# Kernel tuning notes

Hardware: AMD Instinct MI355X
Metric: run time of the kernel (lower is better)

The kernel has to match this reference:

```python
import jax, jax.numpy as jnp
import numpy as np

EPS = 0.05
N = 33554432  # 2**25 annotation steps


def setup_inputs() -> dict:
    key = jax.random.key(0)
    # categories in 1..5 (cat==0 is a no-op skip in the original loop; excluding it
    # keeps the output length static at N+1)
    annotation_series = jax.random.randint(key, (N,), 1, 6, dtype=jnp.int64 if jax.config.jax_enable_x64 else jnp.int32)
    # learned scalar weights of the six Linear(1,1,bias=False) layers, at their init constants
    return {
        "annotation_series": annotation_series,
        "origin_w": jnp.asarray(0.0, jnp.float32),
        "big_decrease_w": jnp.asarray(-0.3, jnp.float32),
        "decrease_w": jnp.asarray(-0.1, jnp.float32),
        "same_w": jnp.asarray(0.0, jnp.float32),
        "increase_w": jnp.asarray(0.1, jnp.float32),
        "big_increase_w": jnp.asarray(0.3, jnp.float32),
    }


def _change_table(origin_w, bd, d, s, inc, bi):
    sg = jax.lax.stop_gradient  # clamp bounds came from .item() in torch -> detached
    c1 = jnp.minimum(bd, sg(jnp.minimum(0.0, d))) - EPS                 # big decrease
    c2 = jnp.clip(d, sg(bd) + EPS, 0.0 - EPS)                           # decrease
    c3 = s                                                              # same
    c4 = jnp.clip(inc, 0.0 + EPS, sg(bi) - EPS)                         # increase
    c5 = jnp.maximum(bi, sg(jnp.maximum(0.0, inc)) + EPS)               # big increase
    zero = jnp.zeros_like(c1)  # cat 0 unused (inputs restricted to 1..5)
    return jnp.stack([zero, c1, c2, c3, c4, c5])  # [6]


def reference(annotation_series, origin_w, big_decrease_w, decrease_w, same_w, increase_w, big_increase_w):
    table = _change_table(origin_w, big_decrease_w, decrease_w, same_w, increase_w, big_increase_w)
    changes = table[annotation_series]                    # [N] gather from 6-entry LUT
    series = origin_w + jnp.cumsum(changes)               # [N] inclusive prefix sum
    return jnp.concatenate([origin_w[None], series])      # [N+1]
```

## Files before the change

kernel.cpp:

```cpp
#include <hip/hip_runtime.h>

#define EPS_C 0.05f
#define BLOCK 256
#define SUBT 2
#define CHUNK (SUBT * 4096)
#define CHUNK2 2048

typedef int i4 __attribute__((ext_vector_type(4)));

__device__ __forceinline__ void build_table(const float* bd_p, const float* d_p,
                                            const float* s_p, const float* inc_p,
                                            const float* bi_p, float* cs) {
  if (threadIdx.x == 0) {
    float bd = *bd_p, d = *d_p, s = *s_p, inc = *inc_p, bi = *bi_p;
    cs[0] = 0.0f;
    cs[1] = fminf(bd, fminf(0.0f, d)) - EPS_C;
    cs[2] = fminf(fmaxf(d, bd + EPS_C), -EPS_C);
    cs[3] = s;
    cs[4] = fminf(fmaxf(inc, EPS_C), bi - EPS_C);
    cs[5] = fmaxf(bi, fmaxf(0.0f, inc) + EPS_C);
    cs[6] = 0.0f; cs[7] = 0.0f;
  }
}

__global__ __launch_bounds__(BLOCK) void k_reduce_pack(
    const int* __restrict__ ann, const float* bd, const float* d,
    const float* s, const float* inc, const float* bi,
    uint2* __restrict__ packed, float* __restrict__ coarse,
    float* __restrict__ fine) {
  __shared__ float cs[8];
  __shared__ float wsum[SUBT * 4];
  build_table(bd, d, s, inc, bi, cs);
  __syncthreads();

  const int b = blockIdx.x, t = threadIdx.x;
  const int lane = t & 63, wid = t >> 6;
  const i4* in4 = (const i4*)(ann + (size_t)b * CHUNK);

#pragma unroll
  for (int j = 0; j < SUBT; ++j) {
    unsigned int w0 = 0u, w1 = 0u;
    float sum = 0.0f;
#pragma unroll
    for (int i = 0; i < 4; ++i) {
      i4 v = __builtin_nontemporal_load(&in4[j * 1024 + t * 4 + i]);
      sum += cs[v.x] + cs[v.y] + cs[v.z] + cs[v.w];
      unsigned int nib = (unsigned)v.x | ((unsigned)v.y << 4) |
                         ((unsigned)v.z << 8) | ((unsigned)v.w << 12);
      if (i < 2) w0 |= nib << ((i & 1) * 16);
      else       w1 |= nib << ((i & 1) * 16);
    }
    packed[(size_t)b * (SUBT * BLOCK) + j * BLOCK + t] = make_uint2(w0, w1);
#pragma unroll
    for (int off = 32; off >= 1; off >>= 1) sum += __shfl_down(sum, off, 64);
    if (lane == 0) {
      fine[b * (SUBT * 4) + j * 4 + wid] = sum;
      wsum[j * 4 + wid] = sum;
    }
  }
  __syncthreads();
  if (t == 0) {
    float tot = 0.0f;
#pragma unroll
    for (int i = 0; i < SUBT * 4; ++i) tot += wsum[i];
    coarse[b] = tot;
  }
}

__global__ __launch_bounds__(BLOCK) void k_scan_out(
    const unsigned short* __restrict__ uspack, const float* __restrict__ coarse,
    const float* __restrict__ fine, const float* __restrict__ origin,
    const float* bd, const float* d, const float* s, const float* inc,
    const float* bi, float* __restrict__ out, int nb2, int nbc) {
  __shared__ float cs[8];
  __shared__ float wsum[BLOCK / 64];
  __shared__ float s_base;
  build_table(bd, d, s, inc, bi, cs);
  __syncthreads();

  const int b2 = blockIdx.x, t = threadIdx.x;
  const int lane = t & 63, wid = t >> 6;
  const int cb = b2 >> 2;
  const int fcnt = 2 * (b2 & 3);

  unsigned short us0 = uspack[(size_t)b2 * 512 + t];
  unsigned short us1 = uspack[(size_t)b2 * 512 + 256 + t];

  float p = 0.0f;
  for (int i = t; i < cb; i += BLOCK) p += coarse[i];
  if (t < fcnt) p += fine[cb * 8 + t];
#pragma unroll
  for (int off = 32; off >= 1; off >>= 1) p += __shfl_down(p, off, 64);
  if (lane == 0) wsum[wid] = p;
  __syncthreads();
  if (t == 0) s_base = *origin + wsum[0] + wsum[1] + wsum[2] + wsum[3];
  __syncthreads();

  float carry = s_base;
  unsigned short usv[2] = {us0, us1};
#pragma unroll
  for (int r = 0; r < 2; ++r) {
    const unsigned short us = usv[r];
    float v0 = cs[us & 0xF], v1 = cs[(us >> 4) & 0xF];
    float v2 = cs[(us >> 8) & 0xF], v3 = cs[(us >> 12) & 0xF];
    float run = v0 + v1 + v2 + v3;

    float x = run;
#pragma unroll
    for (int off = 1; off < 64; off <<= 1) {
      float y = __shfl_up(x, off, 64);
      if (lane >= off) x += y;
    }
    __syncthreads();
    if (lane == 63) wsum[wid] = x;
    __syncthreads();
    float wexcl = 0.0f, tot = 0.0f;
#pragma unroll
    for (int i = 0; i < BLOCK / 64; ++i) {
      float wv = wsum[i];
      if (i < wid) wexcl += wv;
      tot += wv;
    }
    const float off0 = carry + wexcl + (x - run);

    float4 o;
    o.x = off0;
    o.y = off0 + v0;
    o.z = off0 + v0 + v1;
    o.w = off0 + v0 + v1 + v2;
    ((float4*)(out + (size_t)b2 * CHUNK2 + r * 1024))[t] = o;
    carry += tot;

    if (b2 == nb2 - 1 && t == BLOCK - 1 && r == 1)
      out[(size_t)nb2 * CHUNK2] = off0 + run;
  }
}

extern "C" void kernel_launch(void* const* d_in, const int* in_sizes, int n_in,
                              void* d_out, int out_size, void* d_ws, size_t ws_size,
                              hipStream_t stream) {
  const int*   ann    = (const int*)d_in[0];
  const float* origin = (const float*)d_in[1];
  const float* bd     = (const float*)d_in[2];
  const float* dw     = (const float*)d_in[3];
  const float* sw     = (const float*)d_in[4];
  const float* inc    = (const float*)d_in[5];
  const float* bi     = (const float*)d_in[6];
  float* out = (float*)d_out;

  const int N   = in_sizes[0];
  const int nbc = N / CHUNK;
  const int nb2 = N / CHUNK2;

  float* coarse = (float*)d_ws;
  float* fine   = (float*)((char*)d_ws + 65536);
  uint2* packed = (uint2*)((char*)d_ws + 262144);

  k_reduce_pack<<<nbc, BLOCK, 0, stream>>>(ann, bd, dw, sw, inc, bi,
                                           packed, coarse, fine);
  k_scan_out<<<nb2, BLOCK, 0, stream>>>((const unsigned short*)packed, coarse,
                                        fine, origin, bd, dw, sw, inc, bi,
                                        out, nb2, nbc);
}
```

Before: 264.3 us.

## Replace two-pass reduce/scan with single-pass decoupled look-back scan

Replaces the reduce-then-scan pair of kernels with one kernel that takes a dynamic block ticket, computes each 8192-element tile's sum, and publishes aggregate/inclusive descriptors for a wavefront-parallel decoupled look-back. Values stay in registers as packed nibbles, so the workspace round trip and the second pass over coarse/fine partial sums are gone. A small zeroing kernel clears descriptors and the ticket first. The cost is serial dependence through the look-back chain and spinning with s_sleep, plus reliance on agent-scope atomics for ordering.

```diff
diff --git a/kernel.cpp b/kernel.cpp
--- a/kernel.cpp
+++ b/kernel.cpp
@@ -2,137 +2,151 @@
 
 #define EPS_C 0.05f
 #define BLOCK 256
-#define SUBT 2
-#define CHUNK (SUBT * 4096)
-#define CHUNK2 2048
+#define CHUNK 8192
+#define FLAG_AGG 1ull
+#define FLAG_INC 2ull
 
 typedef int i4 __attribute__((ext_vector_type(4)));
+typedef float f4 __attribute__((ext_vector_type(4)));
 
-__device__ __forceinline__ void build_table(const float* bd_p, const float* d_p,
-                                            const float* s_p, const float* inc_p,
-                                            const float* bi_p, float* cs) {
-  if (threadIdx.x == 0) {
-    float bd = *bd_p, d = *d_p, s = *s_p, inc = *inc_p, bi = *bi_p;
-    cs[0] = 0.0f;
-    cs[1] = fminf(bd, fminf(0.0f, d)) - EPS_C;
-    cs[2] = fminf(fmaxf(d, bd + EPS_C), -EPS_C);
-    cs[3] = s;
-    cs[4] = fminf(fmaxf(inc, EPS_C), bi - EPS_C);
-    cs[5] = fmaxf(bi, fmaxf(0.0f, inc) + EPS_C);
-    cs[6] = 0.0f; cs[7] = 0.0f;
-  }
+__global__ void k_zero(unsigned long long* __restrict__ p, int n) {
+  int i = blockIdx.x * blockDim.x + threadIdx.x;
+  if (i < n) p[i] = 0ull;
 }
 
-__global__ __launch_bounds__(BLOCK) void k_reduce_pack(
-    const int* __restrict__ ann, const float* bd, const float* d,
-    const float* s, const float* inc, const float* bi,
-    uint2* __restrict__ packed, float* __restrict__ coarse,
-    float* __restrict__ fine) {
+__global__ __launch_bounds__(BLOCK) void k_scan_lookback(
+    const int* __restrict__ ann, const float* __restrict__ origin,
+    const float* __restrict__ bd, const float* __restrict__ d,
+    const float* __restrict__ s, const float* __restrict__ inc,
+    const float* __restrict__ bi, float* __restrict__ out,
+    unsigned long long* __restrict__ desc, unsigned int* __restrict__ ticket,
+    int nb) {
   __shared__ float cs[8];
-  __shared__ float wsum[SUBT * 4];
-  build_table(bd, d, s, inc, bi, cs);
+  __shared__ float wsum[4];
+  __shared__ float s_carry;
+  __shared__ int s_bid;
+
+  const int t = threadIdx.x;
+  const int lane = t & 63;
+  const int wid = t >> 6;
+
+  if (t == 0) {
+    float vbd = *bd, vd = *d, vs = *s, vi = *inc, vbi = *bi;
+    cs[0] = 0.0f;
+    cs[1] = fminf(vbd, fminf(0.0f, vd)) - EPS_C;
+    cs[2] = fminf(fmaxf(vd, vbd + EPS_C), -EPS_C);
+    cs[3] = vs;
+    cs[4] = fminf(fmaxf(vi, EPS_C), vbi - EPS_C);
+    cs[5] = fmaxf(vbi, fmaxf(0.0f, vi) + EPS_C);
+    cs[6] = 0.0f; cs[7] = 0.0f;
+    s_bid = (int)atomicAdd(ticket, 1u);
+  }
+  __syncthreads();
+  const int bid = s_bid;
+
+  unsigned pk0 = 0, pk1 = 0, pk2 = 0, pk3 = 0;
+  float tsum = 0.0f;
+  const i4* in4 = (const i4*)ann + ((size_t)bid * (CHUNK / 4) + wid * 512 + lane);
+#pragma unroll
+  for (int r = 0; r < 8; ++r) {
+    i4 v = __builtin_nontemporal_load(&in4[r * 64]);
+    tsum += cs[v.x] + cs[v.y] + cs[v.z] + cs[v.w];
+    unsigned nib = (unsigned)v.x | ((unsigned)v.y << 4) |
+                   ((unsigned)v.z << 8) | ((unsigned)v.w << 12);
+    unsigned sh = (unsigned)(r & 1) * 16u;
+    if (r < 2)      pk0 |= nib << sh;
+    else if (r < 4) pk1 |= nib << sh;
+    else if (r < 6) pk2 |= nib << sh;
+    else            pk3 |= nib << sh;
+  }
+#pragma unroll
+  for (int off = 32; off >= 1; off >>= 1) tsum += __shfl_xor(tsum, off, 64);
+  if (lane == 0) wsum[wid] = tsum;
   __syncthreads();
 
-  const int b = blockIdx.x, t = threadIdx.x;
-  const int lane = t & 63, wid = t >> 6;
-  const i4* in4 = (const i4*)(ann + (size_t)b * CHUNK);
-
+  if (wid == 0) {
+    const float total = wsum[0] + wsum[1] + wsum[2] + wsum[3];
+    float excl = 0.0f;
+    if (bid == 0) {
+      if (lane == 0) {
+        __hip_atomic_store(&desc[0],
+            (FLAG_INC << 32) | (unsigned long long)__float_as_uint(total),
+            __ATOMIC_RELEASE, __HIP_MEMORY_SCOPE_AGENT);
+        s_carry = 0.0f;
+      }
+    } else {
+      if (lane == 0)
+        __hip_atomic_store(&desc[bid],
+            (FLAG_AGG << 32) | (unsigned long long)__float_as_uint(total),
+            __ATOMIC_RELEASE, __HIP_MEMORY_SCOPE_AGENT);
+      int look = bid;
+      for (;;) {
+        const int idx = look - 1 - lane;
+        unsigned long long d0 = (idx >= 0)
+            ? __hip_atomic_load(&desc[idx], __ATOMIC_ACQUIRE, __HIP_MEMORY_SCOPE_AGENT)
+            : (FLAG_INC << 32);
+        const unsigned flag = (unsigned)(d0 >> 32);
+        const unsigned long long binc = __ballot(flag == 2u);
+        const unsigned long long bnone = __ballot(flag == 0u);
+        const int fi = binc ? (__ffsll((long long)binc) - 1) : 64;
+        const int fn = bnone ? (__ffsll((long long)bnone) - 1) : 64;
+        if (fi < fn) {
+          float v = (lane <= fi) ? __uint_as_float((unsigned)d0) : 0.0f;
 #pragma unroll
-  for (int j = 0; j < SUBT; ++j) {
-    unsigned int w0 = 0u, w1 = 0u;
-    float sum = 0.0f;
+          for (int off = 32; off >= 1; off >>= 1) v += __shfl_xor(v, off, 64);
+          excl += v;
+          break;
+        }
+        if (fn > 0) {
+          float v = (lane < fn) ? __uint_as_float((unsigned)d0) : 0.0f;
 #pragma unroll
-    for (int i = 0; i < 4; ++i) {
-      i4 v = __builtin_nontemporal_load(&in4[j * 1024 + t * 4 + i]);
-      sum += cs[v.x] + cs[v.y] + cs[v.z] + cs[v.w];
-      unsigned int nib = (unsigned)v.x | ((unsigned)v.y << 4) |
-                         ((unsigned)v.z << 8) | ((unsigned)v.w << 12);
-      if (i < 2) w0 |= nib << ((i & 1) * 16);
-      else       w1 |= nib << ((i & 1) * 16);
+          for (int off = 32; off >= 1; off >>= 1) v += __shfl_xor(v, off, 64);
+          excl += v;
+          look -= fn;
+        } else {
+          __builtin_amdgcn_s_sleep(1);
+        }
+      }
+      if (lane == 0) {
+        __hip_atomic_store(&desc[bid],
+            (FLAG_INC << 32) | (unsigned long long)__float_as_uint(excl + total),
+            __ATOMIC_RELEASE, __HIP_MEMORY_SCOPE_AGENT);
+        s_carry = excl;
+      }
     }
-    packed[(size_t)b * (SUBT * BLOCK) + j * BLOCK + t] = make_uint2(w0, w1);
-#pragma unroll
-    for (int off = 32; off >= 1; off >>= 1) sum += __shfl_down(sum, off, 64);
-    if (lane == 0) {
-      fine[b * (SUBT * 4) + j * 4 + wid] = sum;
-      wsum[j * 4 + wid] = sum;
-    }
+    if (lane == 0 && bid == nb - 1)
+      out[(size_t)nb * CHUNK] = *origin + excl + total;
   }
   __syncthreads();
-  if (t == 0) {
-    float tot = 0.0f;
+
+  float c = *origin + s_carry;
+  if (wid > 0) c += wsum[0];
+  if (wid > 1) c += wsum[1];
+  if (wid > 2) c += wsum[2];
+  float* ob = out + (size_t)bid * CHUNK + wid * 2048 + lane * 4;
 #pragma unroll
-    for (int i = 0; i < SUBT * 4; ++i) tot += wsum[i];
-    coarse[b] = tot;
-  }
-}
-
-__global__ __launch_bounds__(BLOCK) void k_scan_out(
-    const unsigned short* __restrict__ uspack, const float* __restrict__ coarse,
-    const float* __restrict__ fine, const float* __restrict__ origin,
-    const float* bd, const float* d, const float* s, const float* inc,
-    const float* bi, float* __restrict__ out, int nb2, int nbc) {
-  __shared__ float cs[8];
-  __shared__ float wsum[BLOCK / 64];
-  __shared__ float s_base;
-  build_table(bd, d, s, inc, bi, cs);
-  __syncthreads();
-
-  const int b2 = blockIdx.x, t = threadIdx.x;
-  const int lane = t & 63, wid = t >> 6;
-  const int cb = b2 >> 2;
-  const int fcnt = 2 * (b2 & 3);
-
-  unsigned short us0 = uspack[(size_t)b2 * 512 + t];
-  unsigned short us1 = uspack[(size_t)b2 * 512 + 256 + t];
-
-  float p = 0.0f;
-  for (int i = t; i < cb; i += BLOCK) p += coarse[i];
-  if (t < fcnt) p += fine[cb * 8 + t];
-#pragma unroll
-  for (int off = 32; off >= 1; off >>= 1) p += __shfl_down(p, off, 64);
-  if (lane == 0) wsum[wid] = p;
-  __syncthreads();
-  if (t == 0) s_base = *origin + wsum[0] + wsum[1] + wsum[2] + wsum[3];
-  __syncthreads();
-
-  float carry = s_base;
-  unsigned short usv[2] = {us0, us1};
-#pragma unroll
-  for (int r = 0; r < 2; ++r) {
-    const unsigned short us = usv[r];
-    float v0 = cs[us & 0xF], v1 = cs[(us >> 4) & 0xF];
-    float v2 = cs[(us >> 8) & 0xF], v3 = cs[(us >> 12) & 0xF];
-    float run = v0 + v1 + v2 + v3;
-
-    float x = run;
+  for (int r = 0; r < 8; ++r) {
+    const unsigned pkr = (r < 2) ? pk0 : (r < 4) ? pk1 : (r < 6) ? pk2 : pk3;
+    const unsigned nib = (pkr >> ((r & 1) * 16)) & 0xFFFFu;
+    const float v0 = cs[nib & 0xFu];
+    const float v1 = cs[(nib >> 4) & 0xFu];
+    const float v2 = cs[(nib >> 8) & 0xFu];
+    const float v3 = cs[(nib >> 12) & 0xFu];
+    const float s4 = v0 + v1 + v2 + v3;
+    float x = s4;
 #pragma unroll
     for (int off = 1; off < 64; off <<= 1) {
       float y = __shfl_up(x, off, 64);
       if (lane >= off) x += y;
     }
-    __syncthreads();
-    if (lane == 63) wsum[wid] = x;
-    __syncthreads();
-    float wexcl = 0.0f, tot = 0.0f;
-#pragma unroll
-    for (int i = 0; i < BLOCK / 64; ++i) {
-      float wv = wsum[i];
-      if (i < wid) wexcl += wv;
-      tot += wv;
-    }
-    const float off0 = carry + wexcl + (x - run);
-
-    float4 o;
+    const float off0 = c + (x - s4);
+    f4 o;
     o.x = off0;
     o.y = off0 + v0;
-    o.z = off0 + v0 + v1;
-    o.w = off0 + v0 + v1 + v2;
-    ((float4*)(out + (size_t)b2 * CHUNK2 + r * 1024))[t] = o;
-    carry += tot;
-
-    if (b2 == nb2 - 1 && t == BLOCK - 1 && r == 1)
-      out[(size_t)nb2 * CHUNK2] = off0 + run;
+    o.z = o.y + v1;
+    o.w = o.z + v2;
+    __builtin_nontemporal_store(o, (f4*)(ob + r * 256));
+    c += __shfl(x, 63, 64);
   }
 }
 
@@ -144,21 +158,17 @@
   const float* bd     = (const float*)d_in[2];
   const float* dw     = (const float*)d_in[3];
   const float* sw     = (const float*)d_in[4];
-  const float* inc    = (const float*)d_in[5];
+  const float* ic     = (const float*)d_in[5];
   const float* bi     = (const float*)d_in[6];
   float* out = (float*)d_out;
 
-  const int N   = in_sizes[0];
-  const int nbc = N / CHUNK;
-  const int nb2 = N / CHUNK2;
+  const int N  = in_sizes[0];
+  const int nb = N / CHUNK;
 
-  float* coarse = (float*)d_ws;
-  float* fine   = (float*)((char*)d_ws + 65536);
-  uint2* packed = (uint2*)((char*)d_ws + 262144);
+  unsigned long long* desc = (unsigned long long*)d_ws;
+  unsigned int* ticket = (unsigned int*)(desc + nb);
 
-  k_reduce_pack<<<nbc, BLOCK, 0, stream>>>(ann, bd, dw, sw, inc, bi,
-                                           packed, coarse, fine);
-  k_scan_out<<<nb2, BLOCK, 0, stream>>>((const unsigned short*)packed, coarse,
-                                        fine, origin, bd, dw, sw, inc, bi,
-                                        out, nb2, nbc);
+  k_zero<<<(nb + 1 + 255) / 256, 256, 0, stream>>>(desc, nb + 1);
+  k_scan_lookback<<<nb, BLOCK, 0, stream>>>(ann, origin, bd, dw, sw, ic, bi,
+                                            out, desc, ticket, nb);
 }
```

New measurement: 701.7 us. 2.66x slower.

## Split scan into reduce, single-block fine prefix scan, and wave-local output pass

Applied to the files above, without the earlier changes.

Replaces the two-kernel scheme, in which every output block re-summed all preceding coarse partials, with three kernels. The first packs the input and writes per-1024-element partial sums. A single 1024-thread block then scans those partials into exclusive prefixes. The output kernel makes each wave independent, with no block barriers, and writes with nontemporal stores. This removes the quadratic prefix reduction and the block syncs, at the cost of an extra launch and a serial single-block middle step.

```diff
diff --git a/kernel.cpp b/kernel.cpp
--- a/kernel.cpp
+++ b/kernel.cpp
@@ -1,12 +1,9 @@
 #include <hip/hip_runtime.h>
 
 #define EPS_C 0.05f
-#define BLOCK 256
-#define SUBT 2
-#define CHUNK (SUBT * 4096)
-#define CHUNK2 2048
 
 typedef int i4 __attribute__((ext_vector_type(4)));
+typedef float f4 __attribute__((ext_vector_type(4)));
 
 __device__ __forceinline__ void build_table(const float* bd_p, const float* d_p,
                                             const float* s_p, const float* inc_p,
@@ -23,116 +20,116 @@
   }
 }
 
-__global__ __launch_bounds__(BLOCK) void k_reduce_pack(
+__global__ __launch_bounds__(256) void k_pack_reduce(
     const int* __restrict__ ann, const float* bd, const float* d,
     const float* s, const float* inc, const float* bi,
-    uint2* __restrict__ packed, float* __restrict__ coarse,
-    float* __restrict__ fine) {
+    unsigned short* __restrict__ pack, float* __restrict__ fine) {
   __shared__ float cs[8];
-  __shared__ float wsum[SUBT * 4];
   build_table(bd, d, s, inc, bi, cs);
   __syncthreads();
-
-  const int b = blockIdx.x, t = threadIdx.x;
-  const int lane = t & 63, wid = t >> 6;
-  const i4* in4 = (const i4*)(ann + (size_t)b * CHUNK);
-
+  const int t = threadIdx.x, lane = t & 63, w = t >> 6, b = blockIdx.x;
+  const size_t ebase = (size_t)b * 8192 + w * 2048;
+  const i4* in4 = (const i4*)ann + (ebase >> 2) + lane;
+  unsigned short* pk = pack + (ebase >> 2) + lane;
+  float fs0 = 0.0f, fs1 = 0.0f;
 #pragma unroll
-  for (int j = 0; j < SUBT; ++j) {
-    unsigned int w0 = 0u, w1 = 0u;
-    float sum = 0.0f;
+  for (int r = 0; r < 8; ++r) {
+    i4 v = __builtin_nontemporal_load(&in4[r * 64]);
+    float e = cs[v.x] + cs[v.y] + cs[v.z] + cs[v.w];
+    if (r < 4) fs0 += e; else fs1 += e;
+    unsigned us = (unsigned)v.x | ((unsigned)v.y << 4) |
+                  ((unsigned)v.z << 8) | ((unsigned)v.w << 12);
+    pk[r * 64] = (unsigned short)us;
+  }
 #pragma unroll
-    for (int i = 0; i < 4; ++i) {
-      i4 v = __builtin_nontemporal_load(&in4[j * 1024 + t * 4 + i]);
-      sum += cs[v.x] + cs[v.y] + cs[v.z] + cs[v.w];
-      unsigned int nib = (unsigned)v.x | ((unsigned)v.y << 4) |
-                         ((unsigned)v.z << 8) | ((unsigned)v.w << 12);
-      if (i < 2) w0 |= nib << ((i & 1) * 16);
-      else       w1 |= nib << ((i & 1) * 16);
-    }
-    packed[(size_t)b * (SUBT * BLOCK) + j * BLOCK + t] = make_uint2(w0, w1);
-#pragma unroll
-    for (int off = 32; off >= 1; off >>= 1) sum += __shfl_down(sum, off, 64);
-    if (lane == 0) {
-      fine[b * (SUBT * 4) + j * 4 + wid] = sum;
-      wsum[j * 4 + wid] = sum;
-    }
+  for (int off = 32; off >= 1; off >>= 1) {
+    fs0 += __shfl_xor(fs0, off, 64);
+    fs1 += __shfl_xor(fs1, off, 64);
   }
-  __syncthreads();
-  if (t == 0) {
-    float tot = 0.0f;
-#pragma unroll
-    for (int i = 0; i < SUBT * 4; ++i) tot += wsum[i];
-    coarse[b] = tot;
+  if (lane == 0) {
+    fine[b * 8 + w * 2 + 0] = fs0;
+    fine[b * 8 + w * 2 + 1] = fs1;
   }
 }
 
-__global__ __launch_bounds__(BLOCK) void k_scan_out(
-    const unsigned short* __restrict__ uspack, const float* __restrict__ coarse,
+__global__ __launch_bounds__(1024) void k_scan_fine(
     const float* __restrict__ fine, const float* __restrict__ origin,
+    float* __restrict__ pref, float* __restrict__ outN) {
+  __shared__ float ws[16];
+  const int t = threadIdx.x, lane = t & 63, w = t >> 6;
+  float v[32];
+  const f4* fv = (const f4*)fine + t * 8;
+  float tot = 0.0f;
+#pragma unroll
+  for (int i = 0; i < 8; ++i) {
+    f4 x = fv[i];
+    v[i * 4 + 0] = x.x; v[i * 4 + 1] = x.y;
+    v[i * 4 + 2] = x.z; v[i * 4 + 3] = x.w;
+    tot += x.x + x.y + x.z + x.w;
+  }
+  float x = tot;
+#pragma unroll
+  for (int off = 1; off < 64; off <<= 1) {
+    float y = __shfl_up(x, off, 64);
+    if (lane >= off) x += y;
+  }
+  if (lane == 63) ws[w] = x;
+  __syncthreads();
+  float wexcl = 0.0f;
+#pragma unroll
+  for (int i = 0; i < 16; ++i) { float wv = ws[i]; if (i < w) wexcl += wv; }
+  float run = *origin + wexcl + (x - tot);
+#pragma unroll
+  for (int i = 0; i < 8; ++i) {
+    f4 o;
+    o.x = run; run += v[i * 4 + 0];
+    o.y = run; run += v[i * 4 + 1];
+    o.z = run; run += v[i * 4 + 2];
+    o.w = run; run += v[i * 4 + 3];
+    ((f4*)pref)[t * 8 + i] = o;
+  }
+  if (t == 1023) *outN = run;
+}
+
+__global__ __launch_bounds__(256) void k_scan_out(
+    const unsigned short* __restrict__ pack, const float* __restrict__ pref,
     const float* bd, const float* d, const float* s, const float* inc,
-    const float* bi, float* __restrict__ out, int nb2, int nbc) {
+    const float* bi, float* __restrict__ out) {
   __shared__ float cs[8];
-  __shared__ float wsum[BLOCK / 64];
-  __shared__ float s_base;
   build_table(bd, d, s, inc, bi, cs);
   __syncthreads();
-
-  const int b2 = blockIdx.x, t = threadIdx.x;
-  const int lane = t & 63, wid = t >> 6;
-  const int cb = b2 >> 2;
-  const int fcnt = 2 * (b2 & 3);
-
-  unsigned short us0 = uspack[(size_t)b2 * 512 + t];
-  unsigned short us1 = uspack[(size_t)b2 * 512 + 256 + t];
-
-  float p = 0.0f;
-  for (int i = t; i < cb; i += BLOCK) p += coarse[i];
-  if (t < fcnt) p += fine[cb * 8 + t];
+  const int t = threadIdx.x, lane = t & 63, w = t >> 6, b = blockIdx.x;
 #pragma unroll
-  for (int off = 32; off >= 1; off >>= 1) p += __shfl_down(p, off, 64);
-  if (lane == 0) wsum[wid] = p;
-  __syncthreads();
-  if (t == 0) s_base = *origin + wsum[0] + wsum[1] + wsum[2] + wsum[3];
-  __syncthreads();
-
-  float carry = s_base;
-  unsigned short usv[2] = {us0, us1};
+  for (int h = 0; h < 2; ++h) {
+    const int u = b * 8 + w * 2 + h;
+    const size_t ebase = (size_t)u * 1024;
+    const unsigned short* pk = pack + (ebase >> 2) + lane;
+    unsigned short us0 = pk[0], us1 = pk[64], us2 = pk[128], us3 = pk[192];
+    float carry = pref[u];
+    unsigned short usv[4] = {us0, us1, us2, us3};
 #pragma unroll
-  for (int r = 0; r < 2; ++r) {
-    const unsigned short us = usv[r];
-    float v0 = cs[us & 0xF], v1 = cs[(us >> 4) & 0xF];
-    float v2 = cs[(us >> 8) & 0xF], v3 = cs[(us >> 12) & 0xF];
-    float run = v0 + v1 + v2 + v3;
-
-    float x = run;
+    for (int r = 0; r < 4; ++r) {
+      const unsigned us = usv[r];
+      const float v0 = cs[us & 0xFu];
+      const float v1 = cs[(us >> 4) & 0xFu];
+      const float v2 = cs[(us >> 8) & 0xFu];
+      const float v3 = cs[(us >> 12) & 0xFu];
+      const float s4 = v0 + v1 + v2 + v3;
+      float x = s4;
 #pragma unroll
-    for (int off = 1; off < 64; off <<= 1) {
-      float y = __shfl_up(x, off, 64);
-      if (lane >= off) x += y;
+      for (int off = 1; off < 64; off <<= 1) {
+        float y = __shfl_up(x, off, 64);
+        if (lane >= off) x += y;
+      }
+      const float off0 = carry + (x - s4);
+      f4 o;
+      o.x = off0;
+      o.y = off0 + v0;
+      o.z = o.y + v1;
+      o.w = o.z + v2;
+      __builtin_nontemporal_store(o, (f4*)(out + ebase + r * 256 + lane * 4));
+      carry += __shfl(x, 63, 64);
     }
-    __syncthreads();
-    if (lane == 63) wsum[wid] = x;
-    __syncthreads();
-    float wexcl = 0.0f, tot = 0.0f;
-#pragma unroll
-    for (int i = 0; i < BLOCK / 64; ++i) {
-      float wv = wsum[i];
-      if (i < wid) wexcl += wv;
-      tot += wv;
-    }
-    const float off0 = carry + wexcl + (x - run);
-
-    float4 o;
-    o.x = off0;
-    o.y = off0 + v0;
-    o.z = off0 + v0 + v1;
-    o.w = off0 + v0 + v1 + v2;
-    ((float4*)(out + (size_t)b2 * CHUNK2 + r * 1024))[t] = o;
-    carry += tot;
-
-    if (b2 == nb2 - 1 && t == BLOCK - 1 && r == 1)
-      out[(size_t)nb2 * CHUNK2] = off0 + run;
   }
 }
 
@@ -144,21 +141,19 @@
   const float* bd     = (const float*)d_in[2];
   const float* dw     = (const float*)d_in[3];
   const float* sw     = (const float*)d_in[4];
-  const float* inc    = (const float*)d_in[5];
+  const float* ic     = (const float*)d_in[5];
   const float* bi     = (const float*)d_in[6];
   float* out = (float*)d_out;
 
   const int N   = in_sizes[0];
-  const int nbc = N / CHUNK;
-  const int nb2 = N / CHUNK2;
+  const int nb  = N / 8192;
+  const int nf  = N / 1024;
 
-  float* coarse = (float*)d_ws;
-  float* fine   = (float*)((char*)d_ws + 65536);
-  uint2* packed = (uint2*)((char*)d_ws + 262144);
+  float* fine = (float*)d_ws;
+  float* pref = fine + nf;
+  unsigned short* pack = (unsigned short*)(pref + nf);
 
-  k_reduce_pack<<<nbc, BLOCK, 0, stream>>>(ann, bd, dw, sw, inc, bi,
-                                           packed, coarse, fine);
-  k_scan_out<<<nb2, BLOCK, 0, stream>>>((const unsigned short*)packed, coarse,
-                                        fine, origin, bd, dw, sw, inc, bi,
-                                        out, nb2, nbc);
+  k_pack_reduce<<<nb, 256, 0, stream>>>(ann, bd, dw, sw, ic, bi, pack, fine);
+  k_scan_fine<<<1, 1024, 0, stream>>>(fine, origin, pref, out + N);
+  k_scan_out<<<nb, 256, 0, stream>>>(pack, pref, bd, dw, sw, ic, bi, out);
 }
```

Result: faster. 248.1 us (-6.1%).
